# Optimization experiments

Measured on AMD Instinct MI355X. Metric: run time of the kernel, lower is better.

The kernel has to match this reference:

```python
import jax, jax.numpy as jnp
import numpy as np

B, Q, K, C, H = 64, 512, 512, 256, 8
HD = C // H  # per-head dim = 32
OUT = 256


def setup_inputs() -> dict:
    key = jax.random.key(0)
    ks = jax.random.split(key, 11)
    s = 0.05
    return {
        "q_data": jax.random.normal(ks[0], (B, Q, C), jnp.float32),
        "m_data": jax.random.normal(ks[1], (B, K, C), jnp.float32),
        "bias": jax.random.normal(ks[2], (B, 1, Q, K), jnp.float32),
        "nonbatched_bias": jax.random.normal(ks[3], (H, Q, K), jnp.float32),
        "query_w": jax.random.normal(ks[4], (C, H, HD), jnp.float32) * s,
        "key_w": jax.random.normal(ks[5], (C, H, HD), jnp.float32) * s,
        "value_w": jax.random.normal(ks[6], (C, H, HD), jnp.float32) * s,
        "gating_w": jax.random.normal(ks[7], (C, H, HD), jnp.float32) * s,
        "gating_b": jnp.ones((H, HD), jnp.float32),
        "output_w": jax.random.normal(ks[8], (H, HD, OUT), jnp.float32) * s,
        "output_b": jnp.zeros((OUT,), jnp.float32),
    }


def reference(q_data, m_data, bias, nonbatched_bias, query_w, key_w, value_w,
              gating_w, gating_b, output_w, output_b):
    key_dim = query_w.shape[-1]
    # projections
    q = jnp.einsum('bqa,ahc->bqhc', q_data, query_w) * key_dim ** (-0.5)
    k = jnp.einsum('bka,ahc->bkhc', m_data, key_w)
    v = jnp.einsum('bka,ahc->bkhc', m_data, value_w)
    # bias-augmented attention logits [b,h,q,k]
    logits = jnp.einsum('bqhc,bkhc->bhqk', q, k) + bias
    logits = logits + nonbatched_bias[None]
    weights = jax.nn.softmax(logits, axis=-1)
    weighted_avg = jnp.einsum('bhqk,bkhc->bqhc', weights, v)
    # sigmoid gating
    gate = jax.nn.sigmoid(jnp.einsum('bqc,chv->bqhv', q_data, gating_w) + gating_b)
    weighted_avg = weighted_avg * gate
    # output projection
    return jnp.einsum('bqhc,hco->bqo', weighted_avg, output_w) + output_b
```

## Files before the change

### kernel.cpp

```cpp
#include <hip/hip_runtime.h>
#include <math.h>

#define Bb 64
#define Qn 512
#define Kn 512
#define Cn 256
#define Hn 8
#define HDn 32
#define OUTn 256

typedef __bf16 bf16_t;
typedef __attribute__((ext_vector_type(4))) __bf16 bf16x4;
typedef __attribute__((ext_vector_type(8))) __bf16 bf16x8;
typedef __attribute__((ext_vector_type(4))) float f32x4;
typedef __attribute__((ext_vector_type(4))) unsigned int u32x4;

__device__ inline bf16_t tob(float f) {
    unsigned int u = __float_as_uint(f);
    u += 0x7fff + ((u >> 16) & 1);
    unsigned short s = (unsigned short)(u >> 16);
    return __builtin_bit_cast(bf16_t, s);
}

__device__ inline void gl_lds16(const void* g, void* l) {
    __builtin_amdgcn_global_load_lds(
        (const __attribute__((address_space(1))) unsigned int*)g,
        (__attribute__((address_space(3))) unsigned int*)l, 16, 0, 0);
}

__global__ __launch_bounds__(256) void prep_weights(
    const float* __restrict__ qw, const float* __restrict__ kw,
    const float* __restrict__ vw, const float* __restrict__ gw,
    const float* __restrict__ ow,
    bf16_t* __restrict__ wtq, bf16_t* __restrict__ wtk,
    bf16_t* __restrict__ wtv, bf16_t* __restrict__ wtg,
    bf16_t* __restrict__ wto)
{
    int tid = blockIdx.x * 256 + threadIdx.x;
    int mat = tid >> 16;
    int rem = tid & 65535;
    int a = rem >> 8;
    int n = rem & 255;
    const float* src = mat == 0 ? qw : mat == 1 ? kw : mat == 2 ? vw : mat == 3 ? gw : ow;
    bf16_t* dst = mat == 0 ? wtq : mat == 1 ? wtk : mat == 2 ? wtv : mat == 3 ? wtg : wto;
    dst[n * 256 + a] = tob(src[a * 256 + n]);
}

#define ALDS_STRIDE 264
__global__ __launch_bounds__(512) void proj_kernel(
    const float* __restrict__ qdata, const float* __restrict__ mdata,
    const bf16_t* __restrict__ wtq, const bf16_t* __restrict__ wtk,
    const bf16_t* __restrict__ wtv, const bf16_t* __restrict__ wtg,
    const float* __restrict__ gating_b,
    bf16_t* __restrict__ qb, bf16_t* __restrict__ kb,
    bf16_t* __restrict__ vTb, bf16_t* __restrict__ gateb)
{
    __shared__ bf16_t alds[64 * ALDS_STRIDE];
    const int side = blockIdx.y;
    const int m0 = blockIdx.x * 64;
    const int tid = threadIdx.x;
    const int lane = tid & 63;
    const int w = tid >> 6;
    const int ch = w >> 2;
    const int ncb = (w & 3) * 64;
    const int c15 = lane & 15;
    const int rgrp = lane >> 4;
    const int kof = rgrp * 8;
    const float* X = side ? mdata : qdata;
    const bf16_t* Wt = side == 0 ? (ch == 0 ? wtq : wtg) : (ch == 0 ? wtk : wtv);
    const bool vout = (side == 1) && (ch == 1);

    #pragma unroll
    for (int i = 0; i < 8; i++) {
        int u = tid + i * 512;
        int row = u >> 6;
        int c4 = u & 63;
        f32x4 a4 = *reinterpret_cast<const f32x4*>(X + (size_t)(m0 + row) * 256 + c4 * 4);
        bf16_t* dst = &alds[row * ALDS_STRIDE + c4 * 4];
        #pragma unroll
        for (int j = 0; j < 4; j++) dst[j] = tob(a4[j]);
    }
    __syncthreads();

    f32x4 acc[4][4] = {};
    #pragma unroll
    for (int kc = 0; kc < 8; kc++) {
        bf16x8 am[4], bn[4];
        #pragma unroll
        for (int i = 0; i < 4; i++)
            am[i] = *reinterpret_cast<const bf16x8*>(&alds[(i * 16 + c15) * ALDS_STRIDE + kc * 32 + kof]);
        #pragma unroll
        for (int j = 0; j < 4; j++)
            bn[j] = *reinterpret_cast<const bf16x8*>(Wt + (ncb + j * 16 + c15) * 256 + kc * 32 + kof);
        #pragma unroll
        for (int i = 0; i < 4; i++)
            #pragma unroll
            for (int j = 0; j < 4; j++) {
                if (vout)
                    acc[i][j] = __builtin_amdgcn_mfma_f32_16x16x32_bf16(bn[j], am[i], acc[i][j], 0, 0, 0);
                else
                    acc[i][j] = __builtin_amdgcn_mfma_f32_16x16x32_bf16(am[i], bn[j], acc[i][j], 0, 0, 0);
            }
    }

    const float scale = 0.17677669529663687f * 1.4426950408889634f;
    if (!vout) {
        #pragma unroll
        for (int j = 0; j < 4; j++) {
            int n = ncb + j * 16 + c15;
            int h = n >> 5, d = n & 31;
            #pragma unroll
            for (int i = 0; i < 4; i++) {
                #pragma unroll
                for (int r = 0; r < 4; r++) {
                    int m = m0 + i * 16 + rgrp * 4 + r;
                    int b = m >> 9, pos = m & 511;
                    float v = acc[i][j][r];
                    size_t idx = (((size_t)(b * Hn + h) * Qn + pos) << 5) + d;
                    if (side == 0) {
                        if (ch == 0) {
                            qb[idx] = tob(v * scale);
                        } else {
                            float g = 1.f / (1.f + __expf(-(v + gating_b[n])));
                            gateb[idx] = tob(g);
                        }
                    } else {
                        kb[idx] = tob(v);
                    }
                }
            }
        }
    } else {
        #pragma unroll
        for (int i = 0; i < 4; i++) {
            int m = m0 + i * 16 + c15;
            int b = m >> 9, pos = m & 511;
            int kk = (pos & ~31) | (((pos >> 3) & 1) << 4) | (((pos >> 2) & 1) << 3)
                   | (((pos >> 4) & 1) << 2) | (pos & 3);
            #pragma unroll
            for (int j = 0; j < 4; j++) {
                #pragma unroll
                for (int r = 0; r < 4; r++) {
                    int n = ncb + j * 16 + rgrp * 4 + r;
                    int h = n >> 5, d = n & 31;
                    vTb[((size_t)(b * Hn + h) * HDn + d) * Kn + kk] = tob(acc[i][j][r]);
                }
            }
        }
    }
}

__global__ __launch_bounds__(256) void attn_kernel(
    const bf16_t* __restrict__ qb, const bf16_t* __restrict__ kb,
    const bf16_t* __restrict__ vTb, const bf16_t* __restrict__ gateb,
    const float* __restrict__ bias, const float* __restrict__ nbias,
    bf16_t* __restrict__ wab)
{
    __shared__ __align__(16) char kvlds[2][8192];
    __shared__ __align__(16) float blds[4][16 * 64];
    const int p = blockIdx.x;
    const int qt = p & 7;
    const int h = (p >> 3) & 7;
    const int b = p >> 6;
    const int lane = threadIdx.x & 63;
    const int wv = threadIdx.x >> 6;
    const int q0 = qt * 64 + wv * 16;
    const int c15 = lane & 15;
    const int rgrp = lane >> 4;
    const int kof = rgrp * 8;

    const bf16_t* qbase = qb + (size_t)(b * Hn + h) * Qn * HDn;
    const bf16_t* kbase = kb + (size_t)(b * Hn + h) * Kn * HDn;
    const bf16_t* vbase = vTb + (size_t)(b * Hn + h) * HDn * Kn;
    const float* bROW = bias + ((size_t)b * Qn + q0) * Kn;
    const float* nROW = nbias + ((size_t)h * Qn + q0) * Kn;
    char* blw = (char*)blds[wv];

    const int krw = (wv << 4) + (lane >> 2);
    const int kcb = (lane & 3) << 4;
    const int vrw = (wv << 3) + (lane >> 3);
    const int vcb = (lane & 7) << 4;
    const size_t ksrc0 = ((size_t)krw << 6) + (size_t)(kcb ^ ((krw & 3) << 4));
    const size_t vsrc0 = ((size_t)vrw << 10) + (size_t)(vcb ^ ((vrw & 7) << 4));

    bf16x8 aq = *reinterpret_cast<const bf16x8*>(qbase + (q0 + c15) * HDn + kof);

    const float LOG2E = 1.4426950408889634f;
    const float NML = -12.f * 1.4426950408889634f;
    const f32x4 zML = {NML, NML, NML, NML};
    f32x4 o[2] = {};
    f32x4 lsv = {0.f, 0.f, 0.f, 0.f};

    f32x4 bs[4];
    #pragma unroll
    for (int u = 0; u < 4; u++) {
        int row = u * 4 + rgrp;
        f32x4 x = *reinterpret_cast<const f32x4*>(bROW + (size_t)row * Kn + c15 * 4);
        f32x4 y = *reinterpret_cast<const f32x4*>(nROW + (size_t)row * Kn + c15 * 4);
        bs[u] = x + y;
    }
    gl_lds16((const char*)kbase + ksrc0, (char*)kvlds[0] + wv * 1024);
    gl_lds16((const char*)vbase + vsrc0, (char*)kvlds[0] + 4096 + wv * 1024);

    #pragma unroll 1
    for (int c = 0; c < 8; c++) {
        const int pb = c & 1;
        #pragma unroll
        for (int u = 0; u < 4; u++) {
            int row = u * 4 + rgrp;
            *reinterpret_cast<f32x4*>(blw + (row << 8) + ((c15 << 4) ^ ((row & 7) << 4))) = bs[u];
        }
        if (c < 7) {
            #pragma unroll
            for (int u = 0; u < 4; u++) {
                int row = u * 4 + rgrp;
                f32x4 x = *reinterpret_cast<const f32x4*>(bROW + (size_t)row * Kn + (c + 1) * 64 + c15 * 4);
                f32x4 y = *reinterpret_cast<const f32x4*>(nROW + (size_t)row * Kn + (c + 1) * 64 + c15 * 4);
                bs[u] = x + y;
            }
        }
        __builtin_amdgcn_sched_barrier(0);
        if (c < 7) asm volatile("s_waitcnt vmcnt(8)" ::: "memory");
        else       asm volatile("s_waitcnt vmcnt(0)" ::: "memory");
        __builtin_amdgcn_s_barrier();
        __builtin_amdgcn_sched_barrier(0);
        if (c < 7) {
            char* dstb = (char*)kvlds[pb ^ 1] + wv * 1024;
            gl_lds16((const char*)kbase + (size_t)((c + 1) << 12) + ksrc0, dstb);
            gl_lds16((const char*)vbase + (size_t)((c + 1) << 7) + vsrc0, dstb + 4096);
        }
        const char* kl = (const char*)kvlds[pb];
        f32x4 sc[4];
        #pragma unroll
        for (int t = 0; t < 4; t++) {
            int kr = t * 16 + c15;
            bf16x8 kf = *reinterpret_cast<const bf16x8*>(kl + (kr << 6) + ((rgrp << 4) ^ ((kr & 3) << 4)));
            sc[t] = __builtin_amdgcn_mfma_f32_16x16x32_bf16(kf, aq, zML, 0, 0, 0);
        }
        f32x4 es[4];
        #pragma unroll
        for (int t = 0; t < 4; t++) {
            f32x4 bb = *reinterpret_cast<const f32x4*>(blw + (c15 << 8) + (((t << 6) | (rgrp << 4)) ^ ((c15 & 7) << 4)));
            #pragma unroll
            for (int r = 0; r < 4; r++)
                es[t][r] = __builtin_amdgcn_exp2f(fmaf(bb[r], LOG2E, sc[t][r]));
            lsv += es[t];
        }
        unsigned int pw[8];
        #pragma unroll
        for (int t = 0; t < 4; t++) {
            asm("v_cvt_pk_bf16_f32 %0, %1, %2" : "=v"(pw[t * 2 + 0]) : "v"(es[t][0]), "v"(es[t][1]));
            asm("v_cvt_pk_bf16_f32 %0, %1, %2" : "=v"(pw[t * 2 + 1]) : "v"(es[t][2]), "v"(es[t][3]));
        }
        u32x4 a0 = {pw[0], pw[1], pw[2], pw[3]};
        u32x4 a1 = {pw[4], pw[5], pw[6], pw[7]};
        bf16x8 pa0 = __builtin_bit_cast(bf16x8, a0);
        bf16x8 pa1 = __builtin_bit_cast(bf16x8, a1);
        #pragma unroll
        for (int sub = 0; sub < 2; sub++) {
            bf16x8 ap = sub == 0 ? pa0 : pa1;
            #pragma unroll
            for (int nt = 0; nt < 2; nt++) {
                int vr = nt * 16 + c15;
                bf16x8 bv = *reinterpret_cast<const bf16x8*>(kl + 4096 + (vr << 7)
                                + (((sub << 6) | (rgrp << 4)) ^ ((vr & 7) << 4)));
                o[nt] = __builtin_amdgcn_mfma_f32_16x16x32_bf16(ap, bv, o[nt], 0, 0, 0);
            }
        }
    }

    float lsum = (lsv[0] + lsv[1]) + (lsv[2] + lsv[3]);
    lsum += __shfl_xor(lsum, 16, 64);
    lsum += __shfl_xor(lsum, 32, 64);
    float linv[4];
    #pragma unroll
    for (int r = 0; r < 4; r++)
        linv[r] = 1.f / __shfl(lsum, rgrp * 4 + r, 64);

    const bf16_t* gptr = gateb + (size_t)(b * Hn + h) * Qn * HDn;
    bf16_t* wptr = wab + (size_t)b * Qn * 256;
    const int qg = q0 + rgrp * 4;
    #pragma unroll
    for (int nt = 0; nt < 2; nt++) {
        int d = nt * 16 + c15;
        #pragma unroll
        for (int r = 0; r < 4; r++) {
            float g = (float)gptr[(qg + r) * HDn + d];
            wptr[(qg + r) * 256 + h * 32 + d] = tob(o[nt][r] * linv[r] * g);
        }
    }
}

__global__ __launch_bounds__(256) void outproj_kernel(
    const bf16_t* __restrict__ wab, const bf16_t* __restrict__ wto,
    const float* __restrict__ outb, float* __restrict__ out)
{
    __shared__ bf16_t alds[64 * ALDS_STRIDE];
    const int m0 = blockIdx.x * 64;
    const int tid = threadIdx.x;
    const int lane = tid & 63;
    const int w = tid >> 6;
    const int ncb = w * 64;
    const int c15 = lane & 15;
    const int rgrp = lane >> 4;
    const int kof = rgrp * 8;

    #pragma unroll
    for (int i = 0; i < 8; i++) {
        int u = tid + i * 256;
        int row = u >> 5;
        int c16 = u & 31;
        bf16x8 a8 = *reinterpret_cast<const bf16x8*>(wab + (size_t)(m0 + row) * 256 + c16 * 8);
        *reinterpret_cast<bf16x8*>(&alds[row * ALDS_STRIDE + c16 * 8]) = a8;
    }
    __syncthreads();

    f32x4 acc[4][4] = {};
    #pragma unroll
    for (int kc = 0; kc < 8; kc++) {
        bf16x8 am[4], bn[4];
        #pragma unroll
        for (int i = 0; i < 4; i++)
            am[i] = *reinterpret_cast<const bf16x8*>(&alds[(i * 16 + c15) * ALDS_STRIDE + kc * 32 + kof]);
        #pragma unroll
        for (int j = 0; j < 4; j++)
            bn[j] = *reinterpret_cast<const bf16x8*>(wto + (ncb + j * 16 + c15) * 256 + kc * 32 + kof);
        #pragma unroll
        for (int i = 0; i < 4; i++)
            #pragma unroll
            for (int j = 0; j < 4; j++)
                acc[i][j] = __builtin_amdgcn_mfma_f32_16x16x32_bf16(am[i], bn[j], acc[i][j], 0, 0, 0);
    }

    #pragma unroll
    for (int j = 0; j < 4; j++) {
        int n = ncb + j * 16 + c15;
        float ob = outb[n];
        #pragma unroll
        for (int i = 0; i < 4; i++) {
            #pragma unroll
            for (int r = 0; r < 4; r++) {
                int m = m0 + i * 16 + rgrp * 4 + r;
                out[(size_t)m * 256 + n] = acc[i][j][r] + ob;
            }
        }
    }
}

extern "C" void kernel_launch(void* const* d_in, const int* in_sizes, int n_in,
                              void* d_out, int out_size, void* d_ws, size_t ws_size,
                              hipStream_t stream) {
    const float* q_data = (const float*)d_in[0];
    const float* m_data = (const float*)d_in[1];
    const float* bias = (const float*)d_in[2];
    const float* nbias = (const float*)d_in[3];
    const float* query_w = (const float*)d_in[4];
    const float* key_w = (const float*)d_in[5];
    const float* value_w = (const float*)d_in[6];
    const float* gating_w = (const float*)d_in[7];
    const float* gating_b = (const float*)d_in[8];
    const float* output_w = (const float*)d_in[9];
    const float* output_b = (const float*)d_in[10];
    float* out = (float*)d_out;

    char* ws = (char*)d_ws;
    const size_t WT = 256 * 256 * sizeof(bf16_t);
    const size_t PROJ = (size_t)Bb * Hn * Qn * HDn;
    bf16_t* wtq = (bf16_t*)(ws);
    bf16_t* wtk = (bf16_t*)(ws + WT);
    bf16_t* wtv = (bf16_t*)(ws + 2 * WT);
    bf16_t* wtg = (bf16_t*)(ws + 3 * WT);
    bf16_t* wto = (bf16_t*)(ws + 4 * WT);
    bf16_t* qb = (bf16_t*)(ws + 5 * WT);
    bf16_t* kb = qb + PROJ;
    bf16_t* vtb = kb + PROJ;
    bf16_t* gateb = vtb + PROJ;
    bf16_t* wab = gateb + PROJ;

    prep_weights<<<1280, 256, 0, stream>>>(query_w, key_w, value_w, gating_w, output_w,
                                           wtq, wtk, wtv, wtg, wto);
    proj_kernel<<<dim3(512, 2), 512, 0, stream>>>(q_data, m_data, wtq, wtk, wtv, wtg,
                                                  gating_b, qb, kb, vtb, gateb);
    attn_kernel<<<4096, 256, 0, stream>>>(qb, kb, vtb, gateb, bias, nbias, wab);
    outproj_kernel<<<512, 256, 0, stream>>>(wab, wto, output_b, out);
}
```

Before: 176.6 us.

## Make attention blocks persistent per (batch, head) with full K/V resident in LDS

The attention kernel now launches one block per (batch, head) instead of one per 64-query tile. Each block loads the full K and V for its head into LDS once (64 KB) and loops over all eight query tiles, so K/V global traffic drops eightfold and the per-chunk barriers go away. Block IDs are remapped so neighbouring blocks use different heads of different batches. The cost is a much smaller grid (512 blocks), more LDS per block which limits occupancy, and no overlap of the initial K/V load with compute. Bias streaming is still the dominant traffic and is unchanged.

```diff
diff --git a/kernel.cpp b/kernel.cpp
--- a/kernel.cpp
+++ b/kernel.cpp
@@ -156,15 +156,16 @@
     const float* __restrict__ bias, const float* __restrict__ nbias,
     bf16_t* __restrict__ wab)
 {
-    __shared__ __align__(16) char kvlds[2][8192];
+    __shared__ __align__(16) char klds[32768];
+    __shared__ __align__(16) char vlds[32768];
     __shared__ __align__(16) float blds[4][16 * 64];
-    const int p = blockIdx.x;
-    const int qt = p & 7;
-    const int h = (p >> 3) & 7;
-    const int b = p >> 6;
-    const int lane = threadIdx.x & 63;
-    const int wv = threadIdx.x >> 6;
-    const int q0 = qt * 64 + wv * 16;
+    const int bid = blockIdx.x;
+    const int p = (bid & 7) * 64 + (bid >> 3);
+    const int h = p & 7;
+    const int b = p >> 3;
+    const int tid = threadIdx.x;
+    const int lane = tid & 63;
+    const int wv = tid >> 6;
     const int c15 = lane & 15;
     const int rgrp = lane >> 4;
     const int kof = rgrp * 8;
@@ -172,121 +173,125 @@
     const bf16_t* qbase = qb + (size_t)(b * Hn + h) * Qn * HDn;
     const bf16_t* kbase = kb + (size_t)(b * Hn + h) * Kn * HDn;
     const bf16_t* vbase = vTb + (size_t)(b * Hn + h) * HDn * Kn;
-    const float* bROW = bias + ((size_t)b * Qn + q0) * Kn;
-    const float* nROW = nbias + ((size_t)h * Qn + q0) * Kn;
     char* blw = (char*)blds[wv];
 
-    const int krw = (wv << 4) + (lane >> 2);
-    const int kcb = (lane & 3) << 4;
-    const int vrw = (wv << 3) + (lane >> 3);
-    const int vcb = (lane & 7) << 4;
-    const size_t ksrc0 = ((size_t)krw << 6) + (size_t)(kcb ^ ((krw & 3) << 4));
-    const size_t vsrc0 = ((size_t)vrw << 10) + (size_t)(vcb ^ ((vrw & 7) << 4));
-
-    bf16x8 aq = *reinterpret_cast<const bf16x8*>(qbase + (q0 + c15) * HDn + kof);
+    #pragma unroll
+    for (int i = 0; i < 8; i++) {
+        int gr = i * 64 + (tid >> 2);
+        size_t ksrc = ((size_t)gr << 6) + (size_t)(((tid & 3) << 4) ^ ((gr & 3) << 4));
+        gl_lds16((const char*)kbase + ksrc, &klds[i * 4096 + wv * 1024]);
+        int d = i * 4 + wv;
+        size_t vsrc = ((size_t)d << 10) + (size_t)((lane << 4) ^ ((d & 7) << 4));
+        gl_lds16((const char*)vbase + vsrc, &vlds[i * 4096 + wv * 1024]);
+    }
+    asm volatile("s_waitcnt vmcnt(0)" ::: "memory");
+    __builtin_amdgcn_s_barrier();
 
     const float LOG2E = 1.4426950408889634f;
     const float NML = -12.f * 1.4426950408889634f;
     const f32x4 zML = {NML, NML, NML, NML};
-    f32x4 o[2] = {};
-    f32x4 lsv = {0.f, 0.f, 0.f, 0.f};
 
     f32x4 bs[4];
-    #pragma unroll
-    for (int u = 0; u < 4; u++) {
-        int row = u * 4 + rgrp;
-        f32x4 x = *reinterpret_cast<const f32x4*>(bROW + (size_t)row * Kn + c15 * 4);
-        f32x4 y = *reinterpret_cast<const f32x4*>(nROW + (size_t)row * Kn + c15 * 4);
-        bs[u] = x + y;
-    }
-    gl_lds16((const char*)kbase + ksrc0, (char*)kvlds[0] + wv * 1024);
-    gl_lds16((const char*)vbase + vsrc0, (char*)kvlds[0] + 4096 + wv * 1024);
-
-    #pragma unroll 1
-    for (int c = 0; c < 8; c++) {
-        const int pb = c & 1;
+    {
+        const float* bR = bias + ((size_t)b * Qn + wv * 16) * Kn;
+        const float* nR = nbias + ((size_t)h * Qn + wv * 16) * Kn;
         #pragma unroll
         for (int u = 0; u < 4; u++) {
             int row = u * 4 + rgrp;
-            *reinterpret_cast<f32x4*>(blw + (row << 8) + ((c15 << 4) ^ ((row & 7) << 4))) = bs[u];
-        }
-        if (c < 7) {
+            f32x4 x = *reinterpret_cast<const f32x4*>(bR + (size_t)row * Kn + c15 * 4);
+            f32x4 y = *reinterpret_cast<const f32x4*>(nR + (size_t)row * Kn + c15 * 4);
+            bs[u] = x + y;
+        }
+    }
+
+    #pragma unroll 1
+    for (int qt = 0; qt < 8; qt++) {
+        const int q0 = qt * 64 + wv * 16;
+        const float* bR = bias + ((size_t)b * Qn + q0) * Kn;
+        const float* nR = nbias + ((size_t)h * Qn + q0) * Kn;
+
+        bf16x8 aq = *reinterpret_cast<const bf16x8*>(qbase + (q0 + c15) * HDn + kof);
+        f32x4 o[2] = {};
+        f32x4 lsv = {0.f, 0.f, 0.f, 0.f};
+
+        #pragma unroll 1
+        for (int c = 0; c < 8; c++) {
             #pragma unroll
             for (int u = 0; u < 4; u++) {
                 int row = u * 4 + rgrp;
-                f32x4 x = *reinterpret_cast<const f32x4*>(bROW + (size_t)row * Kn + (c + 1) * 64 + c15 * 4);
-                f32x4 y = *reinterpret_cast<const f32x4*>(nROW + (size_t)row * Kn + (c + 1) * 64 + c15 * 4);
-                bs[u] = x + y;
-            }
-        }
-        __builtin_amdgcn_sched_barrier(0);
-        if (c < 7) asm volatile("s_waitcnt vmcnt(8)" ::: "memory");
-        else       asm volatile("s_waitcnt vmcnt(0)" ::: "memory");
-        __builtin_amdgcn_s_barrier();
-        __builtin_amdgcn_sched_barrier(0);
-        if (c < 7) {
-            char* dstb = (char*)kvlds[pb ^ 1] + wv * 1024;
-            gl_lds16((const char*)kbase + (size_t)((c + 1) << 12) + ksrc0, dstb);
-            gl_lds16((const char*)vbase + (size_t)((c + 1) << 7) + vsrc0, dstb + 4096);
-        }
-        const char* kl = (const char*)kvlds[pb];
-        f32x4 sc[4];
-        #pragma unroll
-        for (int t = 0; t < 4; t++) {
-            int kr = t * 16 + c15;
-            bf16x8 kf = *reinterpret_cast<const bf16x8*>(kl + (kr << 6) + ((rgrp << 4) ^ ((kr & 3) << 4)));
-            sc[t] = __builtin_amdgcn_mfma_f32_16x16x32_bf16(kf, aq, zML, 0, 0, 0);
-        }
-        f32x4 es[4];
-        #pragma unroll
-        for (int t = 0; t < 4; t++) {
-            f32x4 bb = *reinterpret_cast<const f32x4*>(blw + (c15 << 8) + (((t << 6) | (rgrp << 4)) ^ ((c15 & 7) << 4)));
-            #pragma unroll
-            for (int r = 0; r < 4; r++)
-                es[t][r] = __builtin_amdgcn_exp2f(fmaf(bb[r], LOG2E, sc[t][r]));
-            lsv += es[t];
-        }
-        unsigned int pw[8];
-        #pragma unroll
-        for (int t = 0; t < 4; t++) {
-            asm("v_cvt_pk_bf16_f32 %0, %1, %2" : "=v"(pw[t * 2 + 0]) : "v"(es[t][0]), "v"(es[t][1]));
-            asm("v_cvt_pk_bf16_f32 %0, %1, %2" : "=v"(pw[t * 2 + 1]) : "v"(es[t][2]), "v"(es[t][3]));
-        }
-        u32x4 a0 = {pw[0], pw[1], pw[2], pw[3]};
-        u32x4 a1 = {pw[4], pw[5], pw[6], pw[7]};
-        bf16x8 pa0 = __builtin_bit_cast(bf16x8, a0);
-        bf16x8 pa1 = __builtin_bit_cast(bf16x8, a1);
-        #pragma unroll
-        for (int sub = 0; sub < 2; sub++) {
-            bf16x8 ap = sub == 0 ? pa0 : pa1;
-            #pragma unroll
-            for (int nt = 0; nt < 2; nt++) {
-                int vr = nt * 16 + c15;
-                bf16x8 bv = *reinterpret_cast<const bf16x8*>(kl + 4096 + (vr << 7)
-                                + (((sub << 6) | (rgrp << 4)) ^ ((vr & 7) << 4)));
-                o[nt] = __builtin_amdgcn_mfma_f32_16x16x32_bf16(ap, bv, o[nt], 0, 0, 0);
-            }
-        }
-    }
-
-    float lsum = (lsv[0] + lsv[1]) + (lsv[2] + lsv[3]);
-    lsum += __shfl_xor(lsum, 16, 64);
-    lsum += __shfl_xor(lsum, 32, 64);
-    float linv[4];
-    #pragma unroll
-    for (int r = 0; r < 4; r++)
-        linv[r] = 1.f / __shfl(lsum, rgrp * 4 + r, 64);
-
-    const bf16_t* gptr = gateb + (size_t)(b * Hn + h) * Qn * HDn;
-    bf16_t* wptr = wab + (size_t)b * Qn * 256;
-    const int qg = q0 + rgrp * 4;
-    #pragma unroll
-    for (int nt = 0; nt < 2; nt++) {
-        int d = nt * 16 + c15;
-        #pragma unroll
-        for (int r = 0; r < 4; r++) {
-            float g = (float)gptr[(qg + r) * HDn + d];
-            wptr[(qg + r) * 256 + h * 32 + d] = tob(o[nt][r] * linv[r] * g);
+                *reinterpret_cast<f32x4*>(blw + (row << 8) + ((c15 << 4) ^ ((row & 7) << 4))) = bs[u];
+            }
+            if (c < 7 || qt < 7) {
+                const float* pbR = (c < 7) ? bR : bR + (size_t)64 * Kn;
+                const float* pnR = (c < 7) ? nR : nR + (size_t)64 * Kn;
+                const int pcol = (c < 7) ? (c + 1) * 64 : 0;
+                #pragma unroll
+                for (int u = 0; u < 4; u++) {
+                    int row = u * 4 + rgrp;
+                    f32x4 x = *reinterpret_cast<const f32x4*>(pbR + (size_t)row * Kn + pcol + c15 * 4);
+                    f32x4 y = *reinterpret_cast<const f32x4*>(pnR + (size_t)row * Kn + pcol + c15 * 4);
+                    bs[u] = x + y;
+                }
+            }
+            asm volatile("" ::: "memory");
+            f32x4 sc[4];
+            #pragma unroll
+            for (int t = 0; t < 4; t++) {
+                int kr = c * 64 + t * 16 + c15;
+                bf16x8 kf = *reinterpret_cast<const bf16x8*>(&klds[(kr << 6) + ((rgrp << 4) ^ ((kr & 3) << 4))]);
+                sc[t] = __builtin_amdgcn_mfma_f32_16x16x32_bf16(kf, aq, zML, 0, 0, 0);
+            }
+            f32x4 es[4];
+            #pragma unroll
+            for (int t = 0; t < 4; t++) {
+                f32x4 bb = *reinterpret_cast<const f32x4*>(blw + (c15 << 8) + (((t << 6) | (rgrp << 4)) ^ ((c15 & 7) << 4)));
+                #pragma unroll
+                for (int r = 0; r < 4; r++)
+                    es[t][r] = __builtin_amdgcn_exp2f(fmaf(bb[r], LOG2E, sc[t][r]));
+                lsv += es[t];
+            }
+            unsigned int pw[8];
+            #pragma unroll
+            for (int t = 0; t < 4; t++) {
+                asm("v_cvt_pk_bf16_f32 %0, %1, %2" : "=v"(pw[t * 2 + 0]) : "v"(es[t][0]), "v"(es[t][1]));
+                asm("v_cvt_pk_bf16_f32 %0, %1, %2" : "=v"(pw[t * 2 + 1]) : "v"(es[t][2]), "v"(es[t][3]));
+            }
+            u32x4 a0 = {pw[0], pw[1], pw[2], pw[3]};
+            u32x4 a1 = {pw[4], pw[5], pw[6], pw[7]};
+            bf16x8 pa0 = __builtin_bit_cast(bf16x8, a0);
+            bf16x8 pa1 = __builtin_bit_cast(bf16x8, a1);
+            #pragma unroll
+            for (int sub = 0; sub < 2; sub++) {
+                bf16x8 ap = sub == 0 ? pa0 : pa1;
+                #pragma unroll
+                for (int nt = 0; nt < 2; nt++) {
+                    int vr = nt * 16 + c15;
+                    bf16x8 bv = *reinterpret_cast<const bf16x8*>(&vlds[(vr << 10) + c * 128
+                                    + ((((sub << 6) | (rgrp << 4)) ^ ((vr & 7) << 4)))]);
+                    o[nt] = __builtin_amdgcn_mfma_f32_16x16x32_bf16(ap, bv, o[nt], 0, 0, 0);
+                }
+            }
+        }
+
+        float lsum = (lsv[0] + lsv[1]) + (lsv[2] + lsv[3]);
+        lsum += __shfl_xor(lsum, 16, 64);
+        lsum += __shfl_xor(lsum, 32, 64);
+        float linv[4];
+        #pragma unroll
+        for (int r = 0; r < 4; r++)
+            linv[r] = 1.f / __shfl(lsum, rgrp * 4 + r, 64);
+
+        const bf16_t* gptr = gateb + (size_t)(b * Hn + h) * Qn * HDn;
+        bf16_t* wptr = wab + (size_t)b * Qn * 256;
+        const int qg = q0 + rgrp * 4;
+        #pragma unroll
+        for (int nt = 0; nt < 2; nt++) {
+            int d = nt * 16 + c15;
+            #pragma unroll
+            for (int r = 0; r < 4; r++) {
+                float g = (float)gptr[(qg + r) * HDn + d];
+                wptr[(qg + r) * 256 + h * 32 + d] = tob(o[nt][r] * linv[r] * g);
+            }
         }
     }
 }
@@ -381,6 +386,6 @@
                                            wtq, wtk, wtv, wtg, wto);
     proj_kernel<<<dim3(512, 2), 512, 0, stream>>>(q_data, m_data, wtq, wtk, wtv, wtg,
                                                   gating_b, qb, kb, vtb, gateb);
-    attn_kernel<<<4096, 256, 0, stream>>>(qb, kb, vtb, gateb, bias, nbias, wab);
+    attn_kernel<<<512, 256, 0, stream>>>(qb, kb, vtb, gateb, bias, nbias, wab);
     outproj_kernel<<<512, 256, 0, stream>>>(wab, wto, output_b, out);
 }
```

New measurement: 230.3 us. 30.4% more time.

## Pre-tile bias tensors into MFMA fragment order before attention

Applied to the files above, without the earlier changes.

Adds a prep kernel that copies the batched bias and head bias into a tiled layout matching the MFMA accumulator fragment order. The attention kernel then reads bias with contiguous 16-byte vector loads straight into registers instead of staging it through shared memory. The goal is to remove the LDS staging and the strided bias reads inside attention. In exchange it adds a full extra read and write of the 64MB bias, plus a workspace requirement, with a fallback path when the workspace is too small.

```diff
diff --git a/kernel.cpp b/kernel.cpp
--- a/kernel.cpp
+++ b/kernel.cpp
@@ -44,6 +44,31 @@
     const float* src = mat == 0 ? qw : mat == 1 ? kw : mat == 2 ? vw : mat == 3 ? gw : ow;
     bf16_t* dst = mat == 0 ? wtq : mat == 1 ? wtk : mat == 2 ? wtv : mat == 3 ? wtg : wto;
     dst[n * 256 + a] = tob(src[a * 256 + n]);
+}
+
+__global__ __launch_bounds__(256) void prep_bias(
+    const float* __restrict__ bias, const float* __restrict__ nbias,
+    float* __restrict__ btile, float* __restrict__ ntile)
+{
+    size_t vid = (size_t)blockIdx.x * 256 + threadIdx.x;
+    const size_t NB = (size_t)64 * 65536;
+    int lane, t, c, q16;
+    if (vid < NB) {
+        lane = vid & 63; t = (vid >> 6) & 3; c = (vid >> 8) & 7; q16 = (vid >> 11) & 31;
+        int b = vid >> 16;
+        int row = q16 * 16 + (lane & 15);
+        int col = c * 64 + t * 16 + (lane >> 4) * 4;
+        f32x4 v = *reinterpret_cast<const f32x4*>(bias + ((size_t)b * Qn + row) * Kn + col);
+        *reinterpret_cast<f32x4*>(btile + vid * 4) = v;
+    } else {
+        size_t nv = vid - NB;
+        lane = nv & 63; t = (nv >> 6) & 3; c = (nv >> 8) & 7; q16 = (nv >> 11) & 31;
+        int h = nv >> 16;
+        int row = q16 * 16 + (lane & 15);
+        int col = c * 64 + t * 16 + (lane >> 4) * 4;
+        f32x4 v = *reinterpret_cast<const f32x4*>(nbias + ((size_t)h * Qn + row) * Kn + col);
+        *reinterpret_cast<f32x4*>(ntile + nv * 4) = v;
+    }
 }
 
 #define ALDS_STRIDE 264
@@ -153,6 +178,129 @@
 __global__ __launch_bounds__(256) void attn_kernel(
     const bf16_t* __restrict__ qb, const bf16_t* __restrict__ kb,
     const bf16_t* __restrict__ vTb, const bf16_t* __restrict__ gateb,
+    const float* __restrict__ btile, const float* __restrict__ ntile,
+    bf16_t* __restrict__ wab)
+{
+    __shared__ __align__(16) char kvlds[2][8192];
+    const int p = blockIdx.x;
+    const int qt = p & 7;
+    const int h = (p >> 3) & 7;
+    const int b = p >> 6;
+    const int lane = threadIdx.x & 63;
+    const int wv = threadIdx.x >> 6;
+    const int q0 = qt * 64 + wv * 16;
+    const int q16 = qt * 4 + wv;
+    const int c15 = lane & 15;
+    const int rgrp = lane >> 4;
+    const int kof = rgrp * 8;
+
+    const bf16_t* qbase = qb + (size_t)(b * Hn + h) * Qn * HDn;
+    const bf16_t* kbase = kb + (size_t)(b * Hn + h) * Kn * HDn;
+    const bf16_t* vbase = vTb + (size_t)(b * Hn + h) * HDn * Kn;
+    const float* btb = btile + (((size_t)b * 32 + q16) << 13) + lane * 4;
+    const float* ntb = ntile + (((size_t)h * 32 + q16) << 13) + lane * 4;
+
+    const int krw = (wv << 4) + (lane >> 2);
+    const int kcb = (lane & 3) << 4;
+    const int vrw = (wv << 3) + (lane >> 3);
+    const int vcb = (lane & 7) << 4;
+    const size_t ksrc0 = ((size_t)krw << 6) + (size_t)(kcb ^ ((krw & 3) << 4));
+    const size_t vsrc0 = ((size_t)vrw << 10) + (size_t)(vcb ^ ((vrw & 7) << 4));
+
+    bf16x8 aq = *reinterpret_cast<const bf16x8*>(qbase + (q0 + c15) * HDn + kof);
+
+    const float NML = -12.f * 1.4426950408889634f;
+    const float LOG2E = 1.4426950408889634f;
+    const f32x4 zML = {NML, NML, NML, NML};
+    f32x4 o[2] = {};
+    f32x4 lsv = {0.f, 0.f, 0.f, 0.f};
+
+    gl_lds16((const char*)kbase + ksrc0, (char*)kvlds[0] + wv * 1024);
+    gl_lds16((const char*)vbase + vsrc0, (char*)kvlds[0] + 4096 + wv * 1024);
+
+    #pragma unroll 1
+    for (int c = 0; c < 8; c++) {
+        const int pb = c & 1;
+        f32x4 bt[4], nt_[4];
+        #pragma unroll
+        for (int t = 0; t < 4; t++) {
+            bt[t]  = *reinterpret_cast<const f32x4*>(btb + c * 1024 + t * 256);
+            nt_[t] = *reinterpret_cast<const f32x4*>(ntb + c * 1024 + t * 256);
+        }
+        __builtin_amdgcn_sched_barrier(0);
+        asm volatile("s_waitcnt vmcnt(8)" ::: "memory");
+        __builtin_amdgcn_s_barrier();
+        __builtin_amdgcn_sched_barrier(0);
+        if (c < 7) {
+            char* dstb = (char*)kvlds[pb ^ 1] + wv * 1024;
+            gl_lds16((const char*)kbase + (size_t)((c + 1) << 12) + ksrc0, dstb);
+            gl_lds16((const char*)vbase + (size_t)((c + 1) << 7) + vsrc0, dstb + 4096);
+        }
+        const char* kl = (const char*)kvlds[pb];
+        f32x4 sc[4];
+        #pragma unroll
+        for (int t = 0; t < 4; t++) {
+            int kr = t * 16 + c15;
+            bf16x8 kf = *reinterpret_cast<const bf16x8*>(kl + (kr << 6) + ((rgrp << 4) ^ ((kr & 3) << 4)));
+            sc[t] = __builtin_amdgcn_mfma_f32_16x16x32_bf16(kf, aq, zML, 0, 0, 0);
+        }
+        f32x4 es[4];
+        #pragma unroll
+        for (int t = 0; t < 4; t++) {
+            f32x4 bb = bt[t] + nt_[t];
+            #pragma unroll
+            for (int r = 0; r < 4; r++)
+                es[t][r] = __builtin_amdgcn_exp2f(fmaf(bb[r], LOG2E, sc[t][r]));
+            lsv += es[t];
+        }
+        unsigned int pw[8];
+        #pragma unroll
+        for (int t = 0; t < 4; t++) {
+            asm("v_cvt_pk_bf16_f32 %0, %1, %2" : "=v"(pw[t * 2 + 0]) : "v"(es[t][0]), "v"(es[t][1]));
+            asm("v_cvt_pk_bf16_f32 %0, %1, %2" : "=v"(pw[t * 2 + 1]) : "v"(es[t][2]), "v"(es[t][3]));
+        }
+        u32x4 a0 = {pw[0], pw[1], pw[2], pw[3]};
+        u32x4 a1 = {pw[4], pw[5], pw[6], pw[7]};
+        bf16x8 pa0 = __builtin_bit_cast(bf16x8, a0);
+        bf16x8 pa1 = __builtin_bit_cast(bf16x8, a1);
+        #pragma unroll
+        for (int sub = 0; sub < 2; sub++) {
+            bf16x8 ap = sub == 0 ? pa0 : pa1;
+            #pragma unroll
+            for (int nt = 0; nt < 2; nt++) {
+                int vr = nt * 16 + c15;
+                bf16x8 bv = *reinterpret_cast<const bf16x8*>(kl + 4096 + (vr << 7)
+                                + (((sub << 6) | (rgrp << 4)) ^ ((vr & 7) << 4)));
+                o[nt] = __builtin_amdgcn_mfma_f32_16x16x32_bf16(ap, bv, o[nt], 0, 0, 0);
+            }
+        }
+    }
+
+    float lsum = (lsv[0] + lsv[1]) + (lsv[2] + lsv[3]);
+    lsum += __shfl_xor(lsum, 16, 64);
+    lsum += __shfl_xor(lsum, 32, 64);
+    float linv[4];
+    #pragma unroll
+    for (int r = 0; r < 4; r++)
+        linv[r] = 1.f / __shfl(lsum, rgrp * 4 + r, 64);
+
+    const bf16_t* gptr = gateb + (size_t)(b * Hn + h) * Qn * HDn;
+    bf16_t* wptr = wab + (size_t)b * Qn * 256;
+    const int qg = q0 + rgrp * 4;
+    #pragma unroll
+    for (int nt = 0; nt < 2; nt++) {
+        int d = nt * 16 + c15;
+        #pragma unroll
+        for (int r = 0; r < 4; r++) {
+            float g = (float)gptr[(qg + r) * HDn + d];
+            wptr[(qg + r) * 256 + h * 32 + d] = tob(o[nt][r] * linv[r] * g);
+        }
+    }
+}
+
+__global__ __launch_bounds__(256) void attn_kernel_fb(
+    const bf16_t* __restrict__ qb, const bf16_t* __restrict__ kb,
+    const bf16_t* __restrict__ vTb, const bf16_t* __restrict__ gateb,
     const float* __restrict__ bias, const float* __restrict__ nbias,
     bf16_t* __restrict__ wab)
 {
@@ -377,10 +525,22 @@
     bf16_t* gateb = vtb + PROJ;
     bf16_t* wab = gateb + PROJ;
 
+    const size_t BASE = 5 * WT + 5 * PROJ * sizeof(bf16_t);
+    const size_t BT_BYTES = (size_t)64 * 65536 * 16;
+    const size_t NT_BYTES = (size_t)8 * 65536 * 16;
+    const size_t NEED = BASE + BT_BYTES + NT_BYTES;
+
     prep_weights<<<1280, 256, 0, stream>>>(query_w, key_w, value_w, gating_w, output_w,
                                            wtq, wtk, wtv, wtg, wto);
     proj_kernel<<<dim3(512, 2), 512, 0, stream>>>(q_data, m_data, wtq, wtk, wtv, wtg,
                                                   gating_b, qb, kb, vtb, gateb);
-    attn_kernel<<<4096, 256, 0, stream>>>(qb, kb, vtb, gateb, bias, nbias, wab);
+    if (ws_size >= NEED) {
+        float* btile = (float*)(ws + BASE);
+        float* ntile = (float*)(ws + BASE + BT_BYTES);
+        prep_bias<<<18432, 256, 0, stream>>>(bias, nbias, btile, ntile);
+        attn_kernel<<<4096, 256, 0, stream>>>(qb, kb, vtb, gateb, btile, ntile, wab);
+    } else {
+        attn_kernel_fb<<<4096, 256, 0, stream>>>(qb, kb, vtb, gateb, bias, nbias, wab);
+    }
     outproj_kernel<<<512, 256, 0, stream>>>(wab, wto, output_b, out);
 }
```

New measurement: 184.4 us. 1.04x slower.

## Pre-tile bias tensors into MFMA layout and stage projection stores through LDS

Applied to the files above, without the earlier changes.

Adds a prep_bias kernel that copies the batched and per-head bias into a tiled layout matching the MFMA output fragment. The attention kernel can then read bias directly into registers and drops its LDS staging of bias. The projection epilogue now stages results through shared memory so that q/k/gate/vT are written with 16-byte vector stores instead of scattered 2-byte stores. The cost is an extra full pass over the 64MB bias plus 8MB nbias (read and written) on every call, and the attention loop loses its one-chunk-ahead prefetch of bias.

```diff
diff --git a/kernel.cpp b/kernel.cpp
--- a/kernel.cpp
+++ b/kernel.cpp
@@ -46,6 +46,31 @@
     dst[n * 256 + a] = tob(src[a * 256 + n]);
 }
 
+__global__ __launch_bounds__(256) void prep_bias(
+    const float* __restrict__ bias, const float* __restrict__ nbias,
+    float* __restrict__ btile, float* __restrict__ ntile)
+{
+    size_t vid = (size_t)blockIdx.x * 256 + threadIdx.x;
+    const size_t NB = (size_t)64 * 65536;
+    int lane, t, c, q16;
+    if (vid < NB) {
+        lane = vid & 63; t = (vid >> 6) & 3; c = (vid >> 8) & 7; q16 = (vid >> 11) & 31;
+        int b = vid >> 16;
+        int row = q16 * 16 + (lane & 15);
+        int col = c * 64 + t * 16 + (lane >> 4) * 4;
+        f32x4 v = *reinterpret_cast<const f32x4*>(bias + ((size_t)b * Qn + row) * Kn + col);
+        *reinterpret_cast<f32x4*>(btile + vid * 4) = v;
+    } else {
+        size_t nv = vid - NB;
+        lane = nv & 63; t = (nv >> 6) & 3; c = (nv >> 8) & 7; q16 = (nv >> 11) & 31;
+        int h = nv >> 16;
+        int row = q16 * 16 + (lane & 15);
+        int col = c * 64 + t * 16 + (lane >> 4) * 4;
+        f32x4 v = *reinterpret_cast<const f32x4*>(nbias + ((size_t)h * Qn + row) * Kn + col);
+        *reinterpret_cast<f32x4*>(ntile + nv * 4) = v;
+    }
+}
+
 #define ALDS_STRIDE 264
 __global__ __launch_bounds__(512) void proj_kernel(
     const float* __restrict__ qdata, const float* __restrict__ mdata,
@@ -55,7 +80,8 @@
     bf16_t* __restrict__ qb, bf16_t* __restrict__ kb,
     bf16_t* __restrict__ vTb, bf16_t* __restrict__ gateb)
 {
-    __shared__ bf16_t alds[64 * ALDS_STRIDE];
+    __shared__ __align__(16) bf16_t smem[20480];
+    bf16_t* alds = smem;
     const int side = blockIdx.y;
     const int m0 = blockIdx.x * 64;
     const int tid = threadIdx.x;
@@ -103,49 +129,74 @@
             }
     }
 
+    __syncthreads();
+    bf16_t* scr = smem + w * 2560;
+
     const float scale = 0.17677669529663687f * 1.4426950408889634f;
+    const int hbase = ncb >> 5;
+    const int posbase = m0 & 511;
+    const int b = m0 >> 9;
+
     if (!vout) {
-        #pragma unroll
-        for (int j = 0; j < 4; j++) {
-            int n = ncb + j * 16 + c15;
-            int h = n >> 5, d = n & 31;
-            #pragma unroll
-            for (int i = 0; i < 4; i++) {
+        bf16_t* dst = side == 0 ? (ch == 0 ? qb : gateb) : kb;
+        #pragma unroll
+        for (int P = 0; P < 2; P++) {
+            #pragma unroll
+            for (int ii = 0; ii < 2; ii++) {
+                int i = P * 2 + ii;
                 #pragma unroll
-                for (int r = 0; r < 4; r++) {
-                    int m = m0 + i * 16 + rgrp * 4 + r;
-                    int b = m >> 9, pos = m & 511;
-                    float v = acc[i][j][r];
-                    size_t idx = (((size_t)(b * Hn + h) * Qn + pos) << 5) + d;
-                    if (side == 0) {
-                        if (ch == 0) {
-                            qb[idx] = tob(v * scale);
-                        } else {
-                            float g = 1.f / (1.f + __expf(-(v + gating_b[n])));
-                            gateb[idx] = tob(g);
+                for (int j = 0; j < 4; j++) {
+                    int n = ncb + j * 16 + c15;
+                    #pragma unroll
+                    for (int r = 0; r < 4; r++) {
+                        float v = acc[i][j][r];
+                        if (side == 0) {
+                            if (ch == 0) v *= scale;
+                            else v = 1.f / (1.f + __expf(-(v + gating_b[n])));
                         }
-                    } else {
-                        kb[idx] = tob(v);
+                        scr[(ii * 16 + rgrp * 4 + r) * 72 + j * 16 + c15] = tob(v);
                     }
                 }
             }
+            asm volatile("" ::: "memory");
+            #pragma unroll
+            for (int v2 = 0; v2 < 4; v2++) {
+                int row = v2 * 8 + (lane >> 3);
+                int col = (lane & 7) * 8;
+                bf16x8 val = *reinterpret_cast<const bf16x8*>(&scr[row * 72 + col]);
+                int pos = posbase + P * 32 + row;
+                int hh = hbase + (col >> 5);
+                int d = col & 31;
+                *reinterpret_cast<bf16x8*>(dst + (((size_t)(b * Hn + hh) * Qn + pos) << 5) + d) = val;
+            }
+            asm volatile("" ::: "memory");
         }
     } else {
         #pragma unroll
-        for (int i = 0; i < 4; i++) {
-            int m = m0 + i * 16 + c15;
-            int b = m >> 9, pos = m & 511;
-            int kk = (pos & ~31) | (((pos >> 3) & 1) << 4) | (((pos >> 2) & 1) << 3)
-                   | (((pos >> 4) & 1) << 2) | (pos & 3);
-            #pragma unroll
-            for (int j = 0; j < 4; j++) {
+        for (int P = 0; P < 2; P++) {
+            #pragma unroll
+            for (int ii = 0; ii < 2; ii++) {
+                int i = P * 2 + ii;
+                int kperm = (((c15 >> 3) & 1) << 4) | (((c15 >> 2) & 1) << 3) | (ii << 2)
+                          | (((c15 >> 1) & 1) << 1) | (c15 & 1);
                 #pragma unroll
-                for (int r = 0; r < 4; r++) {
-                    int n = ncb + j * 16 + rgrp * 4 + r;
-                    int h = n >> 5, d = n & 31;
-                    vTb[((size_t)(b * Hn + h) * HDn + d) * Kn + kk] = tob(acc[i][j][r]);
-                }
-            }
+                for (int j = 0; j < 4; j++)
+                    #pragma unroll
+                    for (int r = 0; r < 4; r++)
+                        scr[(j * 16 + rgrp * 4 + r) * 40 + kperm] = tob(acc[i][j][r]);
+            }
+            asm volatile("" ::: "memory");
+            #pragma unroll
+            for (int u = 0; u < 4; u++) {
+                int nloc = u * 16 + (lane >> 2);
+                int koff = (lane & 3) * 8;
+                bf16x8 val = *reinterpret_cast<const bf16x8*>(&scr[nloc * 40 + koff]);
+                int hh = hbase + (nloc >> 5);
+                int d = nloc & 31;
+                *reinterpret_cast<bf16x8*>(vTb + ((size_t)(b * Hn + hh) * HDn + d) * Kn
+                                           + posbase + P * 32 + koff) = val;
+            }
+            asm volatile("" ::: "memory");
         }
     }
 }
@@ -153,11 +204,10 @@
 __global__ __launch_bounds__(256) void attn_kernel(
     const bf16_t* __restrict__ qb, const bf16_t* __restrict__ kb,
     const bf16_t* __restrict__ vTb, const bf16_t* __restrict__ gateb,
-    const float* __restrict__ bias, const float* __restrict__ nbias,
+    const float* __restrict__ btile, const float* __restrict__ ntile,
     bf16_t* __restrict__ wab)
 {
     __shared__ __align__(16) char kvlds[2][8192];
-    __shared__ __align__(16) float blds[4][16 * 64];
     const int p = blockIdx.x;
     const int qt = p & 7;
     const int h = (p >> 3) & 7;
@@ -165,6 +215,7 @@
     const int lane = threadIdx.x & 63;
     const int wv = threadIdx.x >> 6;
     const int q0 = qt * 64 + wv * 16;
+    const int q16 = qt * 4 + wv;
     const int c15 = lane & 15;
     const int rgrp = lane >> 4;
     const int kof = rgrp * 8;
@@ -172,9 +223,8 @@
     const bf16_t* qbase = qb + (size_t)(b * Hn + h) * Qn * HDn;
     const bf16_t* kbase = kb + (size_t)(b * Hn + h) * Kn * HDn;
     const bf16_t* vbase = vTb + (size_t)(b * Hn + h) * HDn * Kn;
-    const float* bROW = bias + ((size_t)b * Qn + q0) * Kn;
-    const float* nROW = nbias + ((size_t)h * Qn + q0) * Kn;
-    char* blw = (char*)blds[wv];
+    const float* btb = btile + (((size_t)b * 32 + q16) << 13) + lane * 4;
+    const float* ntb = ntile + (((size_t)h * 32 + q16) << 13) + lane * 4;
 
     const int krw = (wv << 4) + (lane >> 2);
     const int kcb = (lane & 3) << 4;
@@ -185,43 +235,26 @@
 
     bf16x8 aq = *reinterpret_cast<const bf16x8*>(qbase + (q0 + c15) * HDn + kof);
 
+    const float NML = -12.f * 1.4426950408889634f;
     const float LOG2E = 1.4426950408889634f;
-    const float NML = -12.f * 1.4426950408889634f;
     const f32x4 zML = {NML, NML, NML, NML};
     f32x4 o[2] = {};
     f32x4 lsv = {0.f, 0.f, 0.f, 0.f};
 
-    f32x4 bs[4];
-    #pragma unroll
-    for (int u = 0; u < 4; u++) {
-        int row = u * 4 + rgrp;
-        f32x4 x = *reinterpret_cast<const f32x4*>(bROW + (size_t)row * Kn + c15 * 4);
-        f32x4 y = *reinterpret_cast<const f32x4*>(nROW + (size_t)row * Kn + c15 * 4);
-        bs[u] = x + y;
-    }
     gl_lds16((const char*)kbase + ksrc0, (char*)kvlds[0] + wv * 1024);
     gl_lds16((const char*)vbase + vsrc0, (char*)kvlds[0] + 4096 + wv * 1024);
 
     #pragma unroll 1
     for (int c = 0; c < 8; c++) {
         const int pb = c & 1;
-        #pragma unroll
-        for (int u = 0; u < 4; u++) {
-            int row = u * 4 + rgrp;
-            *reinterpret_cast<f32x4*>(blw + (row << 8) + ((c15 << 4) ^ ((row & 7) << 4))) = bs[u];
-        }
-        if (c < 7) {
-            #pragma unroll
-            for (int u = 0; u < 4; u++) {
-                int row = u * 4 + rgrp;
-                f32x4 x = *reinterpret_cast<const f32x4*>(bROW + (size_t)row * Kn + (c + 1) * 64 + c15 * 4);
-                f32x4 y = *reinterpret_cast<const f32x4*>(nROW + (size_t)row * Kn + (c + 1) * 64 + c15 * 4);
-                bs[u] = x + y;
-            }
+        f32x4 bt[4], nt_[4];
+        #pragma unroll
+        for (int t = 0; t < 4; t++) {
+            bt[t]  = *reinterpret_cast<const f32x4*>(btb + c * 1024 + t * 256);
+            nt_[t] = *reinterpret_cast<const f32x4*>(ntb + c * 1024 + t * 256);
         }
         __builtin_amdgcn_sched_barrier(0);
-        if (c < 7) asm volatile("s_waitcnt vmcnt(8)" ::: "memory");
-        else       asm volatile("s_waitcnt vmcnt(0)" ::: "memory");
+        asm volatile("s_waitcnt vmcnt(8)" ::: "memory");
         __builtin_amdgcn_s_barrier();
         __builtin_amdgcn_sched_barrier(0);
         if (c < 7) {
@@ -240,7 +273,7 @@
         f32x4 es[4];
         #pragma unroll
         for (int t = 0; t < 4; t++) {
-            f32x4 bb = *reinterpret_cast<const f32x4*>(blw + (c15 << 8) + (((t << 6) | (rgrp << 4)) ^ ((c15 & 7) << 4)));
+            f32x4 bb = bt[t] + nt_[t];
             #pragma unroll
             for (int r = 0; r < 4; r++)
                 es[t][r] = __builtin_amdgcn_exp2f(fmaf(bb[r], LOG2E, sc[t][r]));
@@ -377,10 +410,16 @@
     bf16_t* gateb = vtb + PROJ;
     bf16_t* wab = gateb + PROJ;
 
+    const size_t BASE = 5 * WT + 5 * PROJ * sizeof(bf16_t);
+    const size_t BT_BYTES = (size_t)64 * 65536 * 16;
+    float* btile = (float*)(ws + BASE);
+    float* ntile = (float*)(ws + BASE + BT_BYTES);
+
     prep_weights<<<1280, 256, 0, stream>>>(query_w, key_w, value_w, gating_w, output_w,
                                            wtq, wtk, wtv, wtg, wto);
+    prep_bias<<<18432, 256, 0, stream>>>(bias, nbias, btile, ntile);
     proj_kernel<<<dim3(512, 2), 512, 0, stream>>>(q_data, m_data, wtq, wtk, wtv, wtg,
                                                   gating_b, qb, kb, vtb, gateb);
-    attn_kernel<<<4096, 256, 0, stream>>>(qb, kb, vtb, gateb, bias, nbias, wab);
+    attn_kernel<<<4096, 256, 0, stream>>>(qb, kb, vtb, gateb, btile, ntile, wab);
     outproj_kernel<<<512, 256, 0, stream>>>(wab, wto, output_b, out);
 }
```

Result: slower. 183.2 us (+3.7%).
